# Performance work log

Measured on AMD Instinct MI355X. Metric: run time of the kernel, lower is better.

Reference implementation:

```python
import jax, jax.numpy as jnp
import numpy as np
import math

D_MODEL = 1024
NUM_HEADS = 16
D_K = D_MODEL // NUM_HEADS
SEQ_LEN = 2048
THETA = 10000.0


def _rope_tables(seq_len, d_k, theta):
    # inv_freq over even dims, angles repeated-interleaved to full d_k
    inv_freq = theta ** (-jnp.arange(0, d_k, 2, dtype=jnp.float32) / d_k)  # [d_k/2]
    pos = jnp.arange(seq_len, dtype=jnp.float32)                          # [s]
    angles = pos[:, None] * inv_freq[None, :]                             # [s, d_k/2]
    angles = jnp.repeat(angles, 2, axis=-1)                               # [s, d_k]
    return jnp.cos(angles), jnp.sin(angles)


def _rotate_half(x):
    # interleaved pairs: (x0,x1,x2,x3,...) -> (-x1,x0,-x3,x2,...)
    x_even = x[..., ::2]
    x_odd = x[..., 1::2]
    return jnp.stack([-x_odd, x_even], axis=-1).reshape(x.shape)


def _apply_rope(x, cos, sin):
    # x: [b, h, s, d_k]; cos/sin: [s, d_k]
    return x * cos + _rotate_half(x) * sin


def setup_inputs() -> dict:
    key = jax.random.key(0)
    ks = jax.random.split(key, 5)
    scale = 1.0 / math.sqrt(D_MODEL)
    X = jax.random.normal(ks[0], (2, SEQ_LEN, D_MODEL), dtype=jnp.float32)
    Wq = jax.random.normal(ks[1], (D_MODEL, D_MODEL), dtype=jnp.float32) * scale
    Wk = jax.random.normal(ks[2], (D_MODEL, D_MODEL), dtype=jnp.float32) * scale
    Wv = jax.random.normal(ks[3], (D_MODEL, D_MODEL), dtype=jnp.float32) * scale
    Wo = jax.random.normal(ks[4], (D_MODEL, D_MODEL), dtype=jnp.float32) * scale
    return {"X": X, "Wq": Wq, "Wk": Wk, "Wv": Wv, "Wo": Wo}


def reference(X, Wq, Wk, Wv, Wo):
    b, s, _ = X.shape
    h, dk = NUM_HEADS, D_K

    def proj(W):
        return (X @ W.T).reshape(b, s, h, dk).transpose(0, 2, 1, 3)  # [b,h,s,dk]

    q, k, v = proj(Wq), proj(Wk), proj(Wv)

    cos, sin = _rope_tables(s, dk, THETA)
    q = _apply_rope(q, cos, sin)
    k = _apply_rope(k, cos, sin)

    scores = jnp.einsum('bhid,bhjd->bhij', q, k) / math.sqrt(dk)
    causal = jnp.tril(jnp.ones((s, s), dtype=bool))
    scores = jnp.where(causal[None, None], scores, -jnp.inf)
    probs = jax.nn.softmax(scores, axis=-1)
    attended = jnp.einsum('bhij,bhjd->bhid', probs, v)               # [b,h,s,dk]

    out = attended.transpose(0, 2, 1, 3).reshape(b, s, h * dk)
    return out @ Wo.T
```

## Files before the change

kernel.cpp:

```cpp
#include <hip/hip_runtime.h>
#include <stdint.h>

#define D_MODEL 1024
#define NUM_HEADS 16
#define DK 64
#define SEQ 2048
#define BATCH 2
#define MROWS (BATCH * SEQ)
#define LOG2E 1.4426950408889634f
#define FIXM 14.0f

typedef short bf16x8 __attribute__((ext_vector_type(8)));
typedef float f32x4 __attribute__((ext_vector_type(4)));
typedef float f32x16 __attribute__((ext_vector_type(16)));

__device__ __forceinline__ unsigned short f2bf(float f) {
    unsigned int u = __float_as_uint(f);
    u = (u + 0x7fffu + ((u >> 16) & 1u)) >> 16;
    return (unsigned short)u;
}
__device__ __forceinline__ float bf2f(unsigned short h) {
    return __uint_as_float(((unsigned int)h) << 16);
}
__device__ __forceinline__ void async16(const void* g, void* l) {
    __builtin_amdgcn_global_load_lds(
        (const __attribute__((address_space(1))) void*)g,
        (__attribute__((address_space(3))) void*)l, 16, 0, 0);
}
__device__ __forceinline__ unsigned int cvtpk(float lo, float hi) {
    unsigned int r;
    asm("v_cvt_pk_bf16_f32 %0, %1, %2" : "=v"(r) : "v"(lo), "v"(hi));
    return r;
}
#define SWZ64(row, b) ((((row) * 8) + ((b) ^ ((row) & 7))) * 8)

__global__ void cast_all(const float4* __restrict__ X, const float4* __restrict__ Wq,
                         const float4* __restrict__ Wk, const float4* __restrict__ Wv,
                         const float4* __restrict__ Wo, ushort4* __restrict__ Xb,
                         ushort4* __restrict__ Wqkvb, ushort4* __restrict__ Wob) {
    int i = blockIdx.x * blockDim.x + threadIdx.x;
    const float4* src;
    ushort4* dst;
    int off;
    if (i < 1048576) { src = X; dst = Xb; off = i; }
    else if (i < 1310720) { src = Wq; dst = Wqkvb; off = i - 1048576; }
    else if (i < 1572864) { src = Wk; dst = Wqkvb + 262144; off = i - 1310720; }
    else if (i < 1835008) { src = Wv; dst = Wqkvb + 524288; off = i - 1572864; }
    else { src = Wo; dst = Wob; off = i - 1835008; }
    float4 v = src[off];
    ushort4 o;
    o.x = f2bf(v.x); o.y = f2bf(v.y); o.z = f2bf(v.z); o.w = f2bf(v.w);
    dst[off] = o;
}

template <int TN, int OUT_BF16>
__global__ __launch_bounds__(256) void gemm_tile32(
    const unsigned short* __restrict__ A, const unsigned short* __restrict__ B,
    void* __restrict__ Cout, int M, int N, int K) {
    __shared__ unsigned short As[128 * 64];
    __shared__ unsigned short Bs[TN * 64];
    const int nwg = gridDim.x * gridDim.y;
    const int bid = blockIdx.y * gridDim.x + blockIdx.x;
    const int swz = (bid & 7) * (nwg >> 3) + (bid >> 3);
    const int m0 = (swz / gridDim.x) * 128, n0 = (swz % gridDim.x) * TN;
    const int t = threadIdx.x;
    const int lane = t & 63, wave = t >> 6;
    const int l31 = lane & 31, lh = lane >> 5;
    constexpr int MI = (TN == 128) ? 2 : 1;
    constexpr int NI = 2;
    const int wr = (TN == 128) ? (wave >> 1) * 64 : wave * 32;
    const int wc = (TN == 128) ? (wave & 1) * 64 : 0;

    f32x16 acc[MI][NI];
#pragma unroll
    for (int mi = 0; mi < MI; ++mi)
#pragma unroll
        for (int ni = 0; ni < NI; ++ni)
#pragma unroll
            for (int r = 0; r < 16; ++r) acc[mi][ni][r] = 0.f;

    for (int k0 = 0; k0 < K; k0 += 64) {
#pragma unroll
        for (int i = 0; i < 4; ++i) {
            int ch = i * 256 + t;
            int r = ch >> 3, b = (ch & 7) ^ (r & 7);
            async16(A + (size_t)(m0 + r) * K + k0 + b * 8, (char*)As + ch * 16);
        }
#pragma unroll
        for (int i = 0; i < TN / 32; ++i) {
            int ch = i * 256 + t;
            int r = ch >> 3, b = (ch & 7) ^ (r & 7);
            async16(B + (size_t)(n0 + r) * K + k0 + b * 8, (char*)Bs + ch * 16);
        }
        __syncthreads();
#pragma unroll
        for (int ks = 0; ks < 4; ++ks) {
            bf16x8 af[MI], bfr[NI];
#pragma unroll
            for (int mi = 0; mi < MI; ++mi)
                af[mi] = *(const bf16x8*)&As[SWZ64(wr + mi * 32 + l31, ks * 2 + lh)];
#pragma unroll
            for (int ni = 0; ni < NI; ++ni)
                bfr[ni] = *(const bf16x8*)&Bs[SWZ64(wc + ni * 32 + l31, ks * 2 + lh)];
#pragma unroll
            for (int mi = 0; mi < MI; ++mi)
#pragma unroll
                for (int ni = 0; ni < NI; ++ni)
                    acc[mi][ni] = __builtin_amdgcn_mfma_f32_32x32x16_bf16(
                        af[mi], bfr[ni], acc[mi][ni], 0, 0, 0);
        }
        __syncthreads();
    }
#pragma unroll
    for (int mi = 0; mi < MI; ++mi)
#pragma unroll
        for (int ni = 0; ni < NI; ++ni)
#pragma unroll
            for (int rg = 0; rg < 4; ++rg)
#pragma unroll
                for (int c = 0; c < 4; ++c) {
                    int gm = m0 + wr + mi * 32 + 8 * rg + 4 * lh + c;
                    int gn = n0 + wc + ni * 32 + l31;
                    float v = acc[mi][ni][rg * 4 + c];
                    if (OUT_BF16)
                        ((unsigned short*)Cout)[(size_t)gm * N + gn] = f2bf(v);
                    else
                        ((float*)Cout)[(size_t)gm * N + gn] = v;
                }
}

__global__ __launch_bounds__(256) void rope_vt(const unsigned short* __restrict__ QKV,
                                               unsigned short* __restrict__ Qr,
                                               unsigned short* __restrict__ Kr,
                                               unsigned short* __restrict__ Vt) {
    __shared__ unsigned short T[64][80];
    const int bx = blockIdx.x;
    const int t = threadIdx.x;
    if (bx < 4096) {
        int tid = bx * 256 + t;
        int bs = tid >> 8;
        int p4 = tid & 255;
        int b = bs >> 11, spos = bs & 2047;
        int h = p4 >> 4, dd = (p4 & 15) * 4;
        float sn0, cs0, sn1, cs1;
        {
            float if0 = __expf(-(float)dd * (9.210340371976184f / 64.0f));
            float if1 = __expf(-(float)(dd + 2) * (9.210340371976184f / 64.0f));
            __sincosf((float)spos * if0, &sn0, &cs0);
            __sincosf((float)spos * if1, &sn1, &cs1);
        }
        const float SCQ = 0.125f * LOG2E;
        float cs0q = cs0 * SCQ, sn0q = sn0 * SCQ;
        float cs1q = cs1 * SCQ, sn1q = sn1 * SCQ;
        size_t src = (size_t)bs * 3072 + h * 64 + dd;
        ushort4 qw = *(const ushort4*)&QKV[src];
        ushort4 kw = *(const ushort4*)&QKV[src + 1024];
        ushort4 qo_, ko_;
        float e = bf2f(qw.x), o = bf2f(qw.y);
        qo_.x = f2bf(e * cs0q - o * sn0q); qo_.y = f2bf(o * cs0q + e * sn0q);
        e = bf2f(qw.z); o = bf2f(qw.w);
        qo_.z = f2bf(e * cs1q - o * sn1q); qo_.w = f2bf(o * cs1q + e * sn1q);
        e = bf2f(kw.x); o = bf2f(kw.y);
        ko_.x = f2bf(e * cs0 - o * sn0); ko_.y = f2bf(o * cs0 + e * sn0);
        e = bf2f(kw.z); o = bf2f(kw.w);
        ko_.z = f2bf(e * cs1 - o * sn1); ko_.w = f2bf(o * cs1 + e * sn1);
        size_t qb = (((size_t)(b * NUM_HEADS + h) * SEQ + spos) * DK + dd);
        *(ushort4*)&Qr[qb] = qo_;
        *(ushort4*)&Kr[qb] = ko_;
    } else {
        int idx = bx - 4096;
        const int s0 = (idx & 31) * 64, bh = idx >> 5;
        const int b = bh >> 4, h = bh & 15;
#pragma unroll
        for (int i = 0; i < 2; ++i) {
            int ch = i * 256 + t;
            int row = ch >> 3, bc = ch & 7;
            *(int4*)&T[row][bc * 8] =
                *(const int4*)&QKV[(size_t)(b * SEQ + s0 + row) * 3072 + 2048 + h * 64 + bc * 8];
        }
        __syncthreads();
#pragma unroll
        for (int i = 0; i < 2; ++i) {
            int ch = i * 256 + t;
            int d = ch >> 3, sb = ch & 7;
            unsigned short tmp[8];
#pragma unroll
            for (int j = 0; j < 8; ++j) tmp[j] = T[sb * 8 + j][d];
            *(int4*)&Vt[(size_t)bh * DK * SEQ + (size_t)d * SEQ + s0 + sb * 8] = *(int4*)tmp;
        }
    }
}

__global__ __launch_bounds__(256, 4) void flash_attn13(
    const unsigned short* __restrict__ Qr, const unsigned short* __restrict__ Kr,
    const unsigned short* __restrict__ Vt, unsigned short* __restrict__ Att) {
    __shared__ unsigned short Ks3[3][64 * 64];
    __shared__ unsigned short Vs[2][64 * 64];
    const int bh = blockIdx.x;
    const int qt = 31 - (int)blockIdx.y;
    const int t = threadIdx.x;
    const int lane = t & 63, wave = t >> 6;
    const int l31 = lane & 31, lh = lane >> 5;
    const int wq = wave >> 1, wd = wave & 1;
    const size_t qkbase = (size_t)bh * SEQ * DK;
    const unsigned short* Kg = Kr + qkbase;
    const unsigned short* Vg = Vt + (size_t)bh * DK * SEQ;
    const int qg = qt * 64 + wq * 32 + l31;

    bf16x8 aq[4];
#pragma unroll
    for (int kk = 0; kk < 4; ++kk)
        aq[kk] = *(const bf16x8*)&Qr[qkbase + (size_t)qg * DK + kk * 16 + lh * 8];

    f32x16 acc0, acc1;
#pragma unroll
    for (int r = 0; r < 16; ++r) { acc0[r] = 0.f; acc1[r] = 0.f; }
    float la[4] = {0.f, 0.f, 0.f, 0.f};

#pragma unroll
    for (int i = 0; i < 2; ++i) {
        int ch = i * 256 + t;
        int row = ch >> 3, sb = (ch & 7) ^ (row & 7);
        async16(Kg + (size_t)row * DK + sb * 8, (char*)Ks3[0] + ch * 16);
    }
#pragma unroll
    for (int i = 0; i < 2; ++i) {
        int ch = i * 256 + t;
        int row = ch >> 3, sb = (ch & 7) ^ (row & 7);
        async16(Vg + (size_t)row * SEQ + sb * 8, (char*)Vs[0] + ch * 16);
    }
#pragma unroll
    for (int i = 0; i < 2; ++i) {
        int ch = i * 256 + t;
        int row = ch >> 3, sb = (ch & 7) ^ (row & 7);
        async16(Kg + (size_t)(64 + row) * DK + sb * 8, (char*)Ks3[1] + ch * 16);
    }

    for (int jt = 0; jt <= qt; ++jt) {
        if (jt < qt)
            asm volatile("s_waitcnt vmcnt(2) lgkmcnt(0)" ::: "memory");
        else
            asm volatile("s_waitcnt vmcnt(0) lgkmcnt(0)" ::: "memory");
        __builtin_amdgcn_s_barrier();
        __builtin_amdgcn_sched_barrier(0);

        if (jt + 1 <= qt) {
            const int j1 = (jt + 1) * 64;
#pragma unroll
            for (int i = 0; i < 2; ++i) {
                int ch = i * 256 + t;
                int row = ch >> 3, sb = (ch & 7) ^ (row & 7);
                async16(Vg + (size_t)row * SEQ + j1 + sb * 8,
                        (char*)Vs[(jt + 1) & 1] + ch * 16);
            }
        }
        if (jt + 2 <= qt) {
            const int j2 = (jt + 2) * 64;
#pragma unroll
            for (int i = 0; i < 2; ++i) {
                int ch = i * 256 + t;
                int row = ch >> 3, sb = (ch & 7) ^ (row & 7);
                async16(Kg + (size_t)(j2 + row) * DK + sb * 8,
                        (char*)Ks3[(jt + 2) % 3] + ch * 16);
            }
        }
        const unsigned short* Kt = Ks3[jt % 3];
        const unsigned short* Vtile = Vs[jt & 1];
        const bool diag = (jt == qt);
        if (diag && wd > wq) continue;

        f32x16 s;
#pragma unroll
        for (int r = 0; r < 16; ++r) s[r] = 0.f;
        __builtin_amdgcn_s_setprio(1);
#pragma unroll
        for (int kk = 0; kk < 4; ++kk) {
            bf16x8 kf = *(const bf16x8*)&Kt[SWZ64(wd * 32 + l31, kk * 2 + lh)];
            s = __builtin_amdgcn_mfma_f32_32x32x16_bf16(kf, aq[kk], s, 0, 0, 0);
        }
        __builtin_amdgcn_s_setprio(0);
        if (diag && wd == wq) {
#pragma unroll
            for (int r = 0; r < 16; ++r) {
                int crow = (r & 3) + 8 * (r >> 2) + 4 * lh;
                if (crow > l31) s[r] = -1e30f;
            }
        }

#pragma unroll
        for (int r = 0; r < 16; ++r) {
            s[r] = __builtin_amdgcn_exp2f(s[r] - FIXM);
            la[r & 3] += s[r];
        }

        bf16x8 frA, frB;
        {
            unsigned int u0 = cvtpk(s[0], s[1]), v0 = cvtpk(s[4], s[5]);
            unsigned int u1 = cvtpk(s[2], s[3]), v1 = cvtpk(s[6], s[7]);
            asm("v_permlane32_swap_b32 %0, %1" : "+v"(u0), "+v"(v0));
            asm("v_permlane32_swap_b32 %0, %1" : "+v"(u1), "+v"(v1));
            uint4 w = {u0, u1, v0, v1};
            frA = *(bf16x8*)&w;
            unsigned int u2 = cvtpk(s[8], s[9]), v2 = cvtpk(s[12], s[13]);
            unsigned int u3 = cvtpk(s[10], s[11]), v3 = cvtpk(s[14], s[15]);
            asm("v_permlane32_swap_b32 %0, %1" : "+v"(u2), "+v"(v2));
            asm("v_permlane32_swap_b32 %0, %1" : "+v"(u3), "+v"(v3));
            uint4 w2_ = {u2, u3, v2, v3};
            frB = *(bf16x8*)&w2_;
        }

        __builtin_amdgcn_s_setprio(1);
        {
            bf16x8 vf0 = *(const bf16x8*)&Vtile[SWZ64(l31, (wd * 2 + 0) * 2 + lh)];
            acc0 = __builtin_amdgcn_mfma_f32_32x32x16_bf16(vf0, frA, acc0, 0, 0, 0);
            bf16x8 vf1 = *(const bf16x8*)&Vtile[SWZ64(l31, (wd * 2 + 1) * 2 + lh)];
            acc0 = __builtin_amdgcn_mfma_f32_32x32x16_bf16(vf1, frB, acc0, 0, 0, 0);
            bf16x8 vf2 = *(const bf16x8*)&Vtile[SWZ64(32 + l31, (wd * 2 + 0) * 2 + lh)];
            acc1 = __builtin_amdgcn_mfma_f32_32x32x16_bf16(vf2, frA, acc1, 0, 0, 0);
            bf16x8 vf3 = *(const bf16x8*)&Vtile[SWZ64(32 + l31, (wd * 2 + 1) * 2 + lh)];
            acc1 = __builtin_amdgcn_mfma_f32_32x32x16_bf16(vf3, frB, acc1, 0, 0, 0);
        }
        __builtin_amdgcn_s_setprio(0);
    }

    float lt = (la[0] + la[1]) + (la[2] + la[3]);
    lt += __shfl_xor(lt, 32, 64);
    __syncthreads();
    float* SC = (float*)Ks3;
    float* LS = (float*)Vs;
    if (wd == 0) {
#pragma unroll
        for (int r = 0; r < 16; ++r) SC[(wq * 2 + 1) * 1024 + r * 64 + lane] = acc1[r];
    } else {
#pragma unroll
        for (int r = 0; r < 16; ++r) SC[(wq * 2 + 0) * 1024 + r * 64 + lane] = acc0[r];
    }
    if (lane < 32) LS[wave * 32 + l31] = lt;
    __syncthreads();
    const float rl = 1.0f / (LS[(wq * 2) * 32 + l31] + LS[(wq * 2 + 1) * 32 + l31]);
    float outv[16];
    if (wd == 0) {
#pragma unroll
        for (int r = 0; r < 16; ++r)
            outv[r] = acc0[r] + SC[(wq * 2 + 0) * 1024 + r * 64 + lane];
    } else {
#pragma unroll
        for (int r = 0; r < 16; ++r)
            outv[r] = acc1[r] + SC[(wq * 2 + 1) * 1024 + r * 64 + lane];
    }

    const int b_ = bh >> 4, h_ = bh & 15;
#pragma unroll
    for (int rg = 0; rg < 4; ++rg) {
        ushort4 o;
        o.x = f2bf(outv[rg * 4 + 0] * rl);
        o.y = f2bf(outv[rg * 4 + 1] * rl);
        o.z = f2bf(outv[rg * 4 + 2] * rl);
        o.w = f2bf(outv[rg * 4 + 3] * rl);
        *(ushort4*)&Att[(size_t)(b_ * SEQ + qg) * D_MODEL + h_ * DK + wd * 32 + 8 * rg + 4 * lh] = o;
    }
}

extern "C" void kernel_launch(void* const* d_in, const int* in_sizes, int n_in,
                              void* d_out, int out_size, void* d_ws, size_t ws_size,
                              hipStream_t stream) {
    const float* X = (const float*)d_in[0];
    const float* Wq = (const float*)d_in[1];
    const float* Wk = (const float*)d_in[2];
    const float* Wv = (const float*)d_in[3];
    const float* Wo = (const float*)d_in[4];

    char* ws = (char*)d_ws;
    unsigned short* Xb     = (unsigned short*)(ws + 0);
    unsigned short* Wqkvb  = (unsigned short*)(ws + (8u << 20));
    unsigned short* Wob    = (unsigned short*)(ws + (14u << 20));
    unsigned short* QKVraw = (unsigned short*)(ws + (16u << 20));
    unsigned short* Kr     = (unsigned short*)(ws + (40u << 20));
    unsigned short* Vt     = (unsigned short*)(ws + (48u << 20));
    unsigned short* Qr     = Xb;
    unsigned short* Att    = QKVraw;

    cast_all<<<8192, 256, 0, stream>>>((const float4*)X, (const float4*)Wq,
                                       (const float4*)Wk, (const float4*)Wv,
                                       (const float4*)Wo, (ushort4*)Xb,
                                       (ushort4*)Wqkvb, (ushort4*)Wob);

    gemm_tile32<128, 1><<<dim3(3072 / 128, MROWS / 128), 256, 0, stream>>>(
        Xb, Wqkvb, QKVraw, MROWS, 3072, D_MODEL);

    rope_vt<<<4096 + 1024, 256, 0, stream>>>(QKVraw, Qr, Kr, Vt);

    flash_attn13<<<dim3(BATCH * NUM_HEADS, 32), 256, 0, stream>>>(Qr, Kr, Vt, Att);

    gemm_tile32<64, 0><<<dim3(D_MODEL / 64, MROWS / 128), 256, 0, stream>>>(
        Att, Wob, d_out, MROWS, D_MODEL, D_MODEL);
}
```

Measured before the change: 169.6 us.

## Process 128-key tiles per iteration with each wave pair handling one 64-key half

The flash attention loop now stages 128-key K and V tiles per iteration, and the two column waves each handle a separate 64-key half instead of splitting a single 64-key tile. This halves the number of barriers and loop iterations and gives each wave twice the MFMA work between syncs. In exchange, shared memory doubles and launch bounds drop to 2 blocks per CU, which lowers occupancy. Diagonal masking is restructured, and on odd/even boundaries one wave can sit idle.

```diff
diff --git a/kernel.cpp b/kernel.cpp
--- a/kernel.cpp
+++ b/kernel.cpp
@@ -33,6 +33,7 @@
     return r;
 }
 #define SWZ64(row, b) ((((row) * 8) + ((b) ^ ((row) & 7))) * 8)
+#define VSWZ(row, L) ((((row) * 16) + ((L) ^ ((row) & 7))) * 8)
 
 __global__ void cast_all(const float4* __restrict__ X, const float4* __restrict__ Wq,
                          const float4* __restrict__ Wk, const float4* __restrict__ Wv,
@@ -191,11 +192,11 @@
     }
 }
 
-__global__ __launch_bounds__(256, 4) void flash_attn13(
+__global__ __launch_bounds__(256, 2) void flash_attn14(
     const unsigned short* __restrict__ Qr, const unsigned short* __restrict__ Kr,
     const unsigned short* __restrict__ Vt, unsigned short* __restrict__ Att) {
-    __shared__ unsigned short Ks3[3][64 * 64];
-    __shared__ unsigned short Vs[2][64 * 64];
+    __shared__ unsigned short Ks3[3][128 * 64];
+    __shared__ unsigned short Vs[2][64 * 128];
     const int bh = blockIdx.x;
     const int qt = 31 - (int)blockIdx.y;
     const int t = threadIdx.x;
@@ -206,6 +207,7 @@
     const unsigned short* Kg = Kr + qkbase;
     const unsigned short* Vg = Vt + (size_t)bh * DK * SEQ;
     const int qg = qt * 64 + wq * 32 + l31;
+    const int NIT = (qt >> 1) + 1;
 
     bf16x8 aq[4];
 #pragma unroll
@@ -218,107 +220,156 @@
     float la[4] = {0.f, 0.f, 0.f, 0.f};
 
 #pragma unroll
-    for (int i = 0; i < 2; ++i) {
+    for (int i = 0; i < 4; ++i) {
         int ch = i * 256 + t;
-        int row = ch >> 3, sb = (ch & 7) ^ (row & 7);
-        async16(Kg + (size_t)row * DK + sb * 8, (char*)Ks3[0] + ch * 16);
-    }
-#pragma unroll
-    for (int i = 0; i < 2; ++i) {
+        int row = ch >> 3, b = (ch & 7) ^ (row & 7);
+        async16(Kg + (size_t)row * DK + b * 8, (char*)Ks3[0] + ch * 16);
+    }
+#pragma unroll
+    for (int i = 0; i < 4; ++i) {
         int ch = i * 256 + t;
-        int row = ch >> 3, sb = (ch & 7) ^ (row & 7);
-        async16(Vg + (size_t)row * SEQ + sb * 8, (char*)Vs[0] + ch * 16);
-    }
-#pragma unroll
-    for (int i = 0; i < 2; ++i) {
+        int row = ch >> 4, lc = (ch & 15) ^ (row & 7);
+        async16(Vg + (size_t)row * SEQ + lc * 8, (char*)Vs[0] + ch * 16);
+    }
+#pragma unroll
+    for (int i = 0; i < 4; ++i) {
         int ch = i * 256 + t;
-        int row = ch >> 3, sb = (ch & 7) ^ (row & 7);
-        async16(Kg + (size_t)(64 + row) * DK + sb * 8, (char*)Ks3[1] + ch * 16);
-    }
-
-    for (int jt = 0; jt <= qt; ++jt) {
-        if (jt < qt)
-            asm volatile("s_waitcnt vmcnt(2) lgkmcnt(0)" ::: "memory");
+        int row = ch >> 3, b = (ch & 7) ^ (row & 7);
+        async16(Kg + (size_t)(128 + row) * DK + b * 8, (char*)Ks3[1] + ch * 16);
+    }
+
+    for (int jt2 = 0; jt2 < NIT; ++jt2) {
+        if (jt2 + 1 < NIT)
+            asm volatile("s_waitcnt vmcnt(4) lgkmcnt(0)" ::: "memory");
         else
             asm volatile("s_waitcnt vmcnt(0) lgkmcnt(0)" ::: "memory");
         __builtin_amdgcn_s_barrier();
         __builtin_amdgcn_sched_barrier(0);
 
-        if (jt + 1 <= qt) {
-            const int j1 = (jt + 1) * 64;
-#pragma unroll
-            for (int i = 0; i < 2; ++i) {
+        if (jt2 + 1 < NIT) {
+            const int j1 = (jt2 + 1) * 128;
+#pragma unroll
+            for (int i = 0; i < 4; ++i) {
                 int ch = i * 256 + t;
-                int row = ch >> 3, sb = (ch & 7) ^ (row & 7);
-                async16(Vg + (size_t)row * SEQ + j1 + sb * 8,
-                        (char*)Vs[(jt + 1) & 1] + ch * 16);
-            }
-        }
-        if (jt + 2 <= qt) {
-            const int j2 = (jt + 2) * 64;
-#pragma unroll
-            for (int i = 0; i < 2; ++i) {
+                int row = ch >> 4, lc = (ch & 15) ^ (row & 7);
+                async16(Vg + (size_t)row * SEQ + j1 + lc * 8,
+                        (char*)Vs[(jt2 + 1) & 1] + ch * 16);
+            }
+        }
+        if (jt2 + 2 < NIT) {
+            const int j2 = (jt2 + 2) * 128;
+#pragma unroll
+            for (int i = 0; i < 4; ++i) {
                 int ch = i * 256 + t;
-                int row = ch >> 3, sb = (ch & 7) ^ (row & 7);
-                async16(Kg + (size_t)(j2 + row) * DK + sb * 8,
-                        (char*)Ks3[(jt + 2) % 3] + ch * 16);
-            }
-        }
-        const unsigned short* Kt = Ks3[jt % 3];
-        const unsigned short* Vtile = Vs[jt & 1];
-        const bool diag = (jt == qt);
-        if (diag && wd > wq) continue;
-
-        f32x16 s;
-#pragma unroll
-        for (int r = 0; r < 16; ++r) s[r] = 0.f;
+                int row = ch >> 3, b = (ch & 7) ^ (row & 7);
+                async16(Kg + (size_t)(j2 + row) * DK + b * 8,
+                        (char*)Ks3[(jt2 + 2) % 3] + ch * 16);
+            }
+        }
+        const int jj = 2 * jt2 + wd;
+        if (jj > qt) continue;
+        const unsigned short* Kt = Ks3[jt2 % 3];
+        const unsigned short* Vtile = Vs[jt2 & 1];
+        const bool diag = (jj == qt);
+        const bool live1 = !(diag && wq == 0);
+
+        f32x16 s0, s1;
+#pragma unroll
+        for (int r = 0; r < 16; ++r) { s0[r] = 0.f; s1[r] = 0.f; }
         __builtin_amdgcn_s_setprio(1);
 #pragma unroll
         for (int kk = 0; kk < 4; ++kk) {
-            bf16x8 kf = *(const bf16x8*)&Kt[SWZ64(wd * 32 + l31, kk * 2 + lh)];
-            s = __builtin_amdgcn_mfma_f32_32x32x16_bf16(kf, aq[kk], s, 0, 0, 0);
+            bf16x8 kf0 = *(const bf16x8*)&Kt[SWZ64(wd * 64 + l31, kk * 2 + lh)];
+            s0 = __builtin_amdgcn_mfma_f32_32x32x16_bf16(kf0, aq[kk], s0, 0, 0, 0);
+        }
+        if (live1) {
+#pragma unroll
+            for (int kk = 0; kk < 4; ++kk) {
+                bf16x8 kf1 = *(const bf16x8*)&Kt[SWZ64(wd * 64 + 32 + l31, kk * 2 + lh)];
+                s1 = __builtin_amdgcn_mfma_f32_32x32x16_bf16(kf1, aq[kk], s1, 0, 0, 0);
+            }
         }
         __builtin_amdgcn_s_setprio(0);
-        if (diag && wd == wq) {
+        if (diag) {
+            if (wq == 0) {
+#pragma unroll
+                for (int r = 0; r < 16; ++r) {
+                    int crow = (r & 3) + 8 * (r >> 2) + 4 * lh;
+                    if (crow > l31) s0[r] = -1e30f;
+                }
+            } else {
+#pragma unroll
+                for (int r = 0; r < 16; ++r) {
+                    int crow = (r & 3) + 8 * (r >> 2) + 4 * lh;
+                    if (crow > l31) s1[r] = -1e30f;
+                }
+            }
+        }
+
+#pragma unroll
+        for (int r = 0; r < 16; ++r) {
+            s0[r] = __builtin_amdgcn_exp2f(s0[r] - FIXM);
+            la[r & 3] += s0[r];
+        }
+        if (live1) {
 #pragma unroll
             for (int r = 0; r < 16; ++r) {
-                int crow = (r & 3) + 8 * (r >> 2) + 4 * lh;
-                if (crow > l31) s[r] = -1e30f;
-            }
-        }
-
-#pragma unroll
-        for (int r = 0; r < 16; ++r) {
-            s[r] = __builtin_amdgcn_exp2f(s[r] - FIXM);
-            la[r & 3] += s[r];
-        }
-
-        bf16x8 frA, frB;
+                s1[r] = __builtin_amdgcn_exp2f(s1[r] - FIXM);
+                la[r & 3] += s1[r];
+            }
+        }
+
+        bf16x8 frA, frB, frC, frD;
         {
-            unsigned int u0 = cvtpk(s[0], s[1]), v0 = cvtpk(s[4], s[5]);
-            unsigned int u1 = cvtpk(s[2], s[3]), v1 = cvtpk(s[6], s[7]);
+            unsigned int u0 = cvtpk(s0[0], s0[1]), v0 = cvtpk(s0[4], s0[5]);
+            unsigned int u1 = cvtpk(s0[2], s0[3]), v1 = cvtpk(s0[6], s0[7]);
             asm("v_permlane32_swap_b32 %0, %1" : "+v"(u0), "+v"(v0));
             asm("v_permlane32_swap_b32 %0, %1" : "+v"(u1), "+v"(v1));
             uint4 w = {u0, u1, v0, v1};
             frA = *(bf16x8*)&w;
-            unsigned int u2 = cvtpk(s[8], s[9]), v2 = cvtpk(s[12], s[13]);
-            unsigned int u3 = cvtpk(s[10], s[11]), v3 = cvtpk(s[14], s[15]);
+            unsigned int u2 = cvtpk(s0[8], s0[9]), v2 = cvtpk(s0[12], s0[13]);
+            unsigned int u3 = cvtpk(s0[10], s0[11]), v3 = cvtpk(s0[14], s0[15]);
             asm("v_permlane32_swap_b32 %0, %1" : "+v"(u2), "+v"(v2));
             asm("v_permlane32_swap_b32 %0, %1" : "+v"(u3), "+v"(v3));
             uint4 w2_ = {u2, u3, v2, v3};
             frB = *(bf16x8*)&w2_;
         }
+        if (live1) {
+            unsigned int u0 = cvtpk(s1[0], s1[1]), v0 = cvtpk(s1[4], s1[5]);
+            unsigned int u1 = cvtpk(s1[2], s1[3]), v1 = cvtpk(s1[6], s1[7]);
+            asm("v_permlane32_swap_b32 %0, %1" : "+v"(u0), "+v"(v0));
+            asm("v_permlane32_swap_b32 %0, %1" : "+v"(u1), "+v"(v1));
+            uint4 w = {u0, u1, v0, v1};
+            frC = *(bf16x8*)&w;
+            unsigned int u2 = cvtpk(s1[8], s1[9]), v2 = cvtpk(s1[12], s1[13]);
+            unsigned int u3 = cvtpk(s1[10], s1[11]), v3 = cvtpk(s1[14], s1[15]);
+            asm("v_permlane32_swap_b32 %0, %1" : "+v"(u2), "+v"(v2));
+            asm("v_permlane32_swap_b32 %0, %1" : "+v"(u3), "+v"(v3));
+            uint4 w2_ = {u2, u3, v2, v3};
+            frD = *(bf16x8*)&w2_;
+        }
 
         __builtin_amdgcn_s_setprio(1);
         {
-            bf16x8 vf0 = *(const bf16x8*)&Vtile[SWZ64(l31, (wd * 2 + 0) * 2 + lh)];
-            acc0 = __builtin_amdgcn_mfma_f32_32x32x16_bf16(vf0, frA, acc0, 0, 0, 0);
-            bf16x8 vf1 = *(const bf16x8*)&Vtile[SWZ64(l31, (wd * 2 + 1) * 2 + lh)];
-            acc0 = __builtin_amdgcn_mfma_f32_32x32x16_bf16(vf1, frB, acc0, 0, 0, 0);
-            bf16x8 vf2 = *(const bf16x8*)&Vtile[SWZ64(32 + l31, (wd * 2 + 0) * 2 + lh)];
-            acc1 = __builtin_amdgcn_mfma_f32_32x32x16_bf16(vf2, frA, acc1, 0, 0, 0);
-            bf16x8 vf3 = *(const bf16x8*)&Vtile[SWZ64(32 + l31, (wd * 2 + 1) * 2 + lh)];
-            acc1 = __builtin_amdgcn_mfma_f32_32x32x16_bf16(vf3, frB, acc1, 0, 0, 0);
+            bf16x8 vf;
+            vf = *(const bf16x8*)&Vtile[VSWZ(l31, 8 * wd + 0 + lh)];
+            acc0 = __builtin_amdgcn_mfma_f32_32x32x16_bf16(vf, frA, acc0, 0, 0, 0);
+            vf = *(const bf16x8*)&Vtile[VSWZ(l31, 8 * wd + 2 + lh)];
+            acc0 = __builtin_amdgcn_mfma_f32_32x32x16_bf16(vf, frB, acc0, 0, 0, 0);
+            vf = *(const bf16x8*)&Vtile[VSWZ(32 + l31, 8 * wd + 0 + lh)];
+            acc1 = __builtin_amdgcn_mfma_f32_32x32x16_bf16(vf, frA, acc1, 0, 0, 0);
+            vf = *(const bf16x8*)&Vtile[VSWZ(32 + l31, 8 * wd + 2 + lh)];
+            acc1 = __builtin_amdgcn_mfma_f32_32x32x16_bf16(vf, frB, acc1, 0, 0, 0);
+            if (live1) {
+                vf = *(const bf16x8*)&Vtile[VSWZ(l31, 8 * wd + 4 + lh)];
+                acc0 = __builtin_amdgcn_mfma_f32_32x32x16_bf16(vf, frC, acc0, 0, 0, 0);
+                vf = *(const bf16x8*)&Vtile[VSWZ(l31, 8 * wd + 6 + lh)];
+                acc0 = __builtin_amdgcn_mfma_f32_32x32x16_bf16(vf, frD, acc0, 0, 0, 0);
+                vf = *(const bf16x8*)&Vtile[VSWZ(32 + l31, 8 * wd + 4 + lh)];
+                acc1 = __builtin_amdgcn_mfma_f32_32x32x16_bf16(vf, frC, acc1, 0, 0, 0);
+                vf = *(const bf16x8*)&Vtile[VSWZ(32 + l31, 8 * wd + 6 + lh)];
+                acc1 = __builtin_amdgcn_mfma_f32_32x32x16_bf16(vf, frD, acc1, 0, 0, 0);
+            }
         }
         __builtin_amdgcn_s_setprio(0);
     }
@@ -390,7 +441,7 @@
 
     rope_vt<<<4096 + 1024, 256, 0, stream>>>(QKVraw, Qr, Kr, Vt);
 
-    flash_attn13<<<dim3(BATCH * NUM_HEADS, 32), 256, 0, stream>>>(Qr, Kr, Vt, Att);
+    flash_attn14<<<dim3(BATCH * NUM_HEADS, 32), 256, 0, stream>>>(Qr, Kr, Vt, Att);
 
     gemm_tile32<64, 0><<<dim3(D_MODEL / 64, MROWS / 128), 256, 0, stream>>>(
         Att, Wob, d_out, MROWS, D_MODEL, D_MODEL);
```

After: 173.3 us. 2.2% more time.
